# Kernel optimization log

Hardware: AMD Instinct MI355X
Metric: run time of the kernel (lower is better)

Reference implementation:

```python
import jax, jax.numpy as jnp
import numpy as np

B, L, D, M = 8, 2048, 512, 256
D2, H = 2 * D, 4 * D  # attention d_model, FFN hidden
EPS = 1e-6


def setup_inputs() -> dict:
    key = jax.random.key(0)
    ks = jax.random.split(key, 16)
    s2 = 1.0 / np.sqrt(D2)
    sD = 1.0 / np.sqrt(D)
    sH = 1.0 / np.sqrt(H)
    f32 = jnp.float32
    return {
        "zr": jax.random.normal(ks[0], (B, L, D), f32),
        "zi": jax.random.normal(ks[1], (B, L, D), f32),
        "Wq": jax.random.normal(ks[2], (D2, D2), f32) * s2,
        "Wk": jax.random.normal(ks[3], (D2, D2), f32) * s2,
        "Wv": jax.random.normal(ks[4], (D2, D2), f32) * s2,
        "Wo": jax.random.normal(ks[5], (D2, D2), f32) * s2,
        "Wf": jax.random.normal(ks[6], (M, D2), f32),  # trainable random features (std normal, FAVOR+)
        "b_attn": jnp.zeros((D,), f32),
        "W1r": jax.random.normal(ks[7], (D, H), f32) * sD,
        "W1i": jax.random.normal(ks[8], (D, H), f32) * sD,
        "b1r": jnp.zeros((H,), f32),
        "b1i": jnp.zeros((H,), f32),
        "W2r": jax.random.normal(ks[9], (H, D), f32) * sH,
        "W2i": jax.random.normal(ks[10], (H, D), f32) * sH,
        "b2r": jnp.zeros((D,), f32),
        "b2i": jnp.zeros((D,), f32),
        "b_ffn": jnp.zeros((D,), f32),
    }


def modrelu(xr, xi, b):
    # ModReLU: relu(|z| + b) * z / |z|, per-channel bias b
    mag = jnp.sqrt(xr * xr + xi * xi + EPS)
    s = jax.nn.relu(mag + b) / mag
    return xr * s, xi * s


def _block(zr, zi, Wq, Wk, Wv, Wo, Wf, b_attn,
           W1r, W1i, b1r, b1i, W2r, W2i, b2r, b2i, b_ffn):
    # --- kernelized linear attention on real/imag concat [B,L,2D] ---
    x = jnp.concatenate([zr, zi], axis=-1)
    scl = D2 ** -0.25
    q = (x @ Wq) * scl
    k = (x @ Wk) * scl
    v = x @ Wv
    # FAVOR+ positive features: phi(u) = exp(Wf u - |u|^2/2) / sqrt(m)
    pq = q @ Wf.T - 0.5 * jnp.sum(q * q, axis=-1, keepdims=True)  # [B,L,M]
    pk = k @ Wf.T - 0.5 * jnp.sum(k * k, axis=-1, keepdims=True)
    phi_q = jnp.exp(pq - jax.lax.stop_gradient(jnp.max(pq, axis=-1, keepdims=True))) / np.sqrt(M)
    phi_k = jnp.exp(pk - jax.lax.stop_gradient(jnp.max(pk))) / np.sqrt(M)
    kv = jnp.einsum('blm,bld->bmd', phi_k, v)              # [B,M,2D]
    den = jnp.einsum('blm,bm->bl', phi_q, phi_k.sum(axis=1))  # [B,L]
    y = jnp.einsum('blm,bmd->bld', phi_q, kv) / (den[..., None] + EPS)
    y = y @ Wo
    yr, yi = y[..., :D], y[..., D:]
    # Add & Norm (ModReLU)
    zr, zi = modrelu(zr + yr, zi + yi, b_attn)
    # --- complex FFN: complex Linear -> CReLU -> complex Linear ---
    hr = zr @ W1r - zi @ W1i + b1r
    hi = zr @ W1i + zi @ W1r + b1i
    hr = jax.nn.relu(hr)
    hi = jax.nn.relu(hi)
    fr = hr @ W2r - hi @ W2i + b2r
    fi = hr @ W2i + hi @ W2r + b2i
    # Add & Norm (ModReLU)
    zr, zi = modrelu(zr + fr, zi + fi, b_ffn)
    return jnp.stack([zr, zi], axis=-1)  # [B,L,D,2]


def reference(zr, zi, Wq, Wk, Wv, Wo, Wf, b_attn,
              W1r, W1i, b1r, b1i, W2r, W2i, b2r, b2i, b_ffn):
    return _block(zr, zi, Wq, Wk, Wv, Wo, Wf, b_attn,
                  W1r, W1i, b1r, b1i, W2r, W2i, b2r, b2i, b_ffn)
```

## Files before the change

kernel.cpp:

```cpp
#include <hip/hip_runtime.h>
#include <math.h>

#define B_ 8
#define L_ 2048
#define D_ 512
#define M_ 256
#define D2_ 1024
#define H_ 2048
#define N_ 16384
#define EPS_ 1e-6f

typedef __attribute__((ext_vector_type(8))) short bf16x8;
typedef __attribute__((ext_vector_type(4))) float f32x4;
typedef unsigned short ushort_t;
typedef unsigned int uint_t;

#define WAITCNT_VM8 0x0F78
#define WAITCNT_VM6 0x0F76
#define WAITCNT_VM4 0x0F74
#define WAITCNT_VM0 0x0F70

__device__ __forceinline__ ushort_t f2bf(float f) {
    uint_t u = __float_as_uint(f);
    u += 0x7FFFu + ((u >> 16) & 1u);
    return (ushort_t)(u >> 16);
}
__device__ __forceinline__ float bf2f(ushort_t u) {
    return __uint_as_float(((uint_t)u) << 16);
}
__device__ __forceinline__ void gload_lds16(const void* g, void* l) {
    __builtin_amdgcn_global_load_lds(
        (const __attribute__((address_space(1))) void*)g,
        (__attribute__((address_space(3))) void*)l, 16, 0, 0);
}

__global__ __launch_bounds__(256)
void gemm_mfma(const ushort_t* __restrict__ A, const ushort_t* __restrict__ Bm,
               void* __restrict__ Cp, int K, int lda, int ldb, int ldc,
               long long sA, long long sB, long long sC,
               int epi, float alpha, const float* __restrict__ aux,
               int auxStride, const float* __restrict__ bias, int obf)
{
    __shared__ ushort_t As[4][128 * 32];
    __shared__ ushort_t Bs[4][128 * 32];

    const int bz = blockIdx.z;
    A  += (long long)bz * sA;
    Bm += (long long)bz * sB;
    const int row0 = blockIdx.y * 128;
    const int col0 = blockIdx.x * 128;

    const int tid  = threadIdx.x;
    const int lane = tid & 63;
    const int wave = tid >> 6;
    const int wr = wave >> 1, wc = wave & 1;

    const int srow = tid >> 2;
    const int skol = (((tid & 3) ^ ((tid >> 3) & 3)) * 8);

    f32x4 acc[4][4];
    #pragma unroll
    for (int i = 0; i < 4; ++i)
        #pragma unroll
        for (int j = 0; j < 4; ++j)
            acc[i][j] = (f32x4){0.f, 0.f, 0.f, 0.f};

    const int fr = lane & 15;
    const int fq = lane >> 4;
    const int koff = ((fq ^ ((fr >> 1) & 3))) * 8;

    const int nT = K >> 5;

    auto issue = [&](int t) {
        const int buf = t & 3;
        const int k0 = t << 5;
        gload_lds16(A + (long long)(row0 + srow) * lda + k0 + skol,
                    &As[buf][(wave * 16) * 32]);
        gload_lds16(A + (long long)(row0 + 64 + srow) * lda + k0 + skol,
                    &As[buf][(64 + wave * 16) * 32]);
        gload_lds16(Bm + (long long)(col0 + srow) * ldb + k0 + skol,
                    &Bs[buf][(wave * 16) * 32]);
        gload_lds16(Bm + (long long)(col0 + 64 + srow) * ldb + k0 + skol,
                    &Bs[buf][(64 + wave * 16) * 32]);
    };

    issue(0);
    if (nT > 1) issue(1);
    for (int t = 0; t < nT; ++t) {
        if (t + 2 < nT) {
            issue(t + 2);
            __builtin_amdgcn_s_waitcnt(WAITCNT_VM8);
        } else if (t + 1 < nT) {
            __builtin_amdgcn_s_waitcnt(WAITCNT_VM4);
        } else {
            __builtin_amdgcn_s_waitcnt(WAITCNT_VM0);
        }
        __builtin_amdgcn_s_barrier();

        const int cur = t & 3;
        bf16x8 a[4], b[4];
        #pragma unroll
        for (int i = 0; i < 4; ++i)
            a[i] = *(const bf16x8*)&As[cur][(wr * 64 + i * 16 + fr) * 32 + koff];
        #pragma unroll
        for (int j = 0; j < 4; ++j)
            b[j] = *(const bf16x8*)&Bs[cur][(wc * 64 + j * 16 + fr) * 32 + koff];
        #pragma unroll
        for (int i = 0; i < 4; ++i)
            #pragma unroll
            for (int j = 0; j < 4; ++j)
                acc[i][j] = __builtin_amdgcn_mfma_f32_16x16x32_bf16(
                    a[i], b[j], acc[i][j], 0, 0, 0);
    }

    const int gr0 = row0 + wr * 64;
    const int gc0 = col0 + wc * 64;
    #pragma unroll
    for (int i = 0; i < 4; ++i) {
        #pragma unroll
        for (int r = 0; r < 4; ++r) {
            const int row = gr0 + i * 16 + fq * 4 + r;
            float raux = 0.f;
            if (epi == 1 || epi == 2) raux = aux[(long long)bz * auxStride + row];
            #pragma unroll
            for (int j = 0; j < 4; ++j) {
                const int col = gc0 + j * 16 + fr;
                float v = acc[i][j][r];
                if (epi == 0)      v *= alpha;
                else if (epi == 1) v -= 0.5f * raux;
                else if (epi == 2) v = v / (raux + EPS_);
                else if (epi == 5) v -= 0.5f * aux[(long long)bz * auxStride + col];
                else if (epi == 3) { v += bias[col]; v = v > 0.f ? v : 0.f; }
                else if (epi == 4) v += bias[col];
                const long long off = (long long)bz * sC + (long long)row * ldc + col;
                if (obf) ((ushort_t*)Cp)[off] = f2bf(v);
                else     ((float*)Cp)[off] = v;
            }
        }
    }
}

__global__ __launch_bounds__(512, 2)
void gemm256(const ushort_t* __restrict__ A, const ushort_t* __restrict__ Bm,
             void* __restrict__ Cp, int K, int lda, int ldb, int ldc,
             long long sA, long long sB, long long sC,
             int epi, float alpha, const float* __restrict__ aux,
             int auxStride, const float* __restrict__ bias, int obf,
             int ksplit)
{
    __shared__ ushort_t As[2][256 * 64];
    __shared__ ushort_t Bs[2][256 * 64];

    const int bzf = blockIdx.z;
    const int bz = bzf / ksplit;
    const int kz = bzf - bz * ksplit;
    const int Kh = K / ksplit;

    A  += (long long)bz * sA + (long long)kz * Kh;
    Bm += (long long)bz * sB + (long long)kz * Kh;
    const int row0 = blockIdx.y * 256;
    const int col0 = blockIdx.x * 256;

    const int tid  = threadIdx.x;
    const int lane = tid & 63;
    const int wave = tid >> 6;
    const int wr   = wave >> 2;
    const int wcn  = wave & 3;

    const int rloc  = tid >> 3;
    const int csrc8 = (((tid & 7) ^ (rloc & 7)) << 3);

    const int fr = lane & 15;
    const int fq = lane >> 4;
    const int sw = fr & 7;
    const int c0off = ((fq ^ sw) << 3);
    const int c1off = (((4 | fq) ^ sw) << 3);

    const int nT = Kh >> 6;

    f32x4 acc[8][4];
    #pragma unroll
    for (int i = 0; i < 8; ++i)
        #pragma unroll
        for (int j = 0; j < 4; ++j)
            acc[i][j] = (f32x4){0.f, 0.f, 0.f, 0.f};

    bf16x8 a[4][2];
    bf16x8 b[4][2];

    auto stage = [&](int bufS, int tS, int half) {
        const int k0 = tS << 6;
        const int rh = (half >= 2) ? 1 : 0;
        const bool isA = (half == 0 || half == 3);
        const ushort_t* g = isA
            ? A  + (long long)(row0 + rh * 128 + rloc) * lda + k0 + csrc8
            : Bm + (long long)(col0 + rh * 128 + rloc) * ldb + k0 + csrc8;
        const long long gstep = 64LL * (isA ? lda : ldb);
        ushort_t* l = (isA ? &As[bufS][0] : &Bs[bufS][0])
                      + (rh * 128 + wave * 8) * 64;
        gload_lds16(g, l);
        gload_lds16(g + gstep, l + 64 * 64);
    };

    auto ldsA = [&](int buf, int mh, int i, int koff) -> bf16x8 {
        return *(const bf16x8*)
            &As[buf][(wr * 128 + mh * 64 + i * 16 + fr) * 64 + koff];
    };
    auto ldsB = [&](int buf, int j, int koff) -> bf16x8 {
        return *(const bf16x8*)
            &Bs[buf][(wcn * 64 + j * 16 + fr) * 64 + koff];
    };

    stage(0, 0, 0); stage(0, 0, 1); stage(0, 0, 2); stage(0, 0, 3);
    stage(1, 1, 0); stage(1, 1, 1); stage(1, 1, 2); stage(1, 1, 3);
    __builtin_amdgcn_s_waitcnt(WAITCNT_VM8);
    __builtin_amdgcn_s_barrier();

    auto tile_body = [&](int t, int buf) {
        #pragma unroll
        for (int i = 0; i < 4; ++i) {
            a[i][0] = ldsA(buf, 0, i, c0off);
            a[i][1] = ldsA(buf, 0, i, c1off);
        }
        #pragma unroll
        for (int j = 0; j < 2; ++j) {
            b[j][0] = ldsB(buf, j, c0off);
            b[j][1] = ldsB(buf, j, c1off);
        }
        __builtin_amdgcn_s_barrier();
        asm volatile("s_waitcnt lgkmcnt(0)" ::: "memory");
        __builtin_amdgcn_s_setprio(1);
        #pragma unroll
        for (int i = 0; i < 4; ++i)
            #pragma unroll
            for (int j = 0; j < 2; ++j) {
                acc[i][j] = __builtin_amdgcn_mfma_f32_16x16x32_bf16(
                    a[i][0], b[j][0], acc[i][j], 0, 0, 0);
                acc[i][j] = __builtin_amdgcn_mfma_f32_16x16x32_bf16(
                    a[i][1], b[j][1], acc[i][j], 0, 0, 0);
            }
        __builtin_amdgcn_s_setprio(0);
        __builtin_amdgcn_s_barrier();

        #pragma unroll
        for (int j = 2; j < 4; ++j) {
            b[j][0] = ldsB(buf, j, c0off);
            b[j][1] = ldsB(buf, j, c1off);
        }
        __builtin_amdgcn_s_barrier();
        asm volatile("s_waitcnt lgkmcnt(0)" ::: "memory");
        __builtin_amdgcn_s_setprio(1);
        #pragma unroll
        for (int i = 0; i < 4; ++i)
            #pragma unroll
            for (int j = 2; j < 4; ++j) {
                acc[i][j] = __builtin_amdgcn_mfma_f32_16x16x32_bf16(
                    a[i][0], b[j][0], acc[i][j], 0, 0, 0);
                acc[i][j] = __builtin_amdgcn_mfma_f32_16x16x32_bf16(
                    a[i][1], b[j][1], acc[i][j], 0, 0, 0);
            }
        __builtin_amdgcn_s_setprio(0);
        __builtin_amdgcn_s_barrier();

        #pragma unroll
        for (int i = 0; i < 4; ++i) {
            a[i][0] = ldsA(buf, 1, i, c0off);
            a[i][1] = ldsA(buf, 1, i, c1off);
        }
        if (t + 2 < nT) stage(buf, t + 2, 1);
        __builtin_amdgcn_s_barrier();
        asm volatile("s_waitcnt lgkmcnt(0)" ::: "memory");
        __builtin_amdgcn_s_setprio(1);
        #pragma unroll
        for (int i = 0; i < 4; ++i)
            #pragma unroll
            for (int j = 2; j < 4; ++j) {
                acc[4 + i][j] = __builtin_amdgcn_mfma_f32_16x16x32_bf16(
                    a[i][0], b[j][0], acc[4 + i][j], 0, 0, 0);
                acc[4 + i][j] = __builtin_amdgcn_mfma_f32_16x16x32_bf16(
                    a[i][1], b[j][1], acc[4 + i][j], 0, 0, 0);
            }
        __builtin_amdgcn_s_setprio(0);
        __builtin_amdgcn_s_barrier();

        if (t + 2 < nT) {
            stage(buf, t + 2, 2); stage(buf, t + 2, 0); stage(buf, t + 2, 3);
        }
        __builtin_amdgcn_s_barrier();
        asm volatile("s_waitcnt lgkmcnt(0)" ::: "memory");
        __builtin_amdgcn_s_setprio(1);
        #pragma unroll
        for (int i = 0; i < 4; ++i)
            #pragma unroll
            for (int j = 0; j < 2; ++j) {
                acc[4 + i][j] = __builtin_amdgcn_mfma_f32_16x16x32_bf16(
                    a[i][0], b[j][0], acc[4 + i][j], 0, 0, 0);
                acc[4 + i][j] = __builtin_amdgcn_mfma_f32_16x16x32_bf16(
                    a[i][1], b[j][1], acc[4 + i][j], 0, 0, 0);
            }
        __builtin_amdgcn_s_setprio(0);
        if (t + 2 < nT)      __builtin_amdgcn_s_waitcnt(WAITCNT_VM8);
        else if (t + 1 < nT) __builtin_amdgcn_s_waitcnt(WAITCNT_VM0);
        __builtin_amdgcn_s_barrier();
    };

    for (int t = 0; t < nT; t += 2) {
        tile_body(t, 0);
        tile_body(t + 1, 1);
    }

    const int gr0 = row0 + wr * 128;
    const int gc0 = col0 + wcn * 64;
    #pragma unroll
    for (int i = 0; i < 8; ++i) {
        #pragma unroll
        for (int r = 0; r < 4; ++r) {
            const int row = gr0 + i * 16 + fq * 4 + r;
            float raux = 0.f;
            if (epi == 1 || epi == 2) raux = aux[(long long)bz * auxStride + row];
            #pragma unroll
            for (int j = 0; j < 4; ++j) {
                const int col = gc0 + j * 16 + fr;
                float v = acc[i][j][r];
                const long long off = (long long)bz * sC + (long long)row * ldc + col;
                if (ksplit > 1) {
                    atomicAdd((float*)Cp + off, v * alpha);
                    continue;
                }
                if (epi == 0)      v *= alpha;
                else if (epi == 1) v -= 0.5f * raux;
                else if (epi == 2) v = v / (raux + EPS_);
                else if (epi == 5) v -= 0.5f * aux[(long long)bz * auxStride + col];
                else if (epi == 3) { v += bias[col]; v = v > 0.f ? v : 0.f; }
                else if (epi == 4) v += bias[col];
                if (obf) ((ushort_t*)Cp)[off] = f2bf(v);
                else     ((float*)Cp)[off] = v;
            }
        }
    }
}

__global__ __launch_bounds__(256)
void seed_c(const float* __restrict__ bias, float* __restrict__ C)
{
    const long long t = (long long)blockIdx.x * 256 + threadIdx.x;
    C[t] = bias ? bias[(int)(t & (D2_ - 1))] : 0.f;
}


__global__ __launch_bounds__(256)
void transpose_cvt_sq(const float* __restrict__ W, ushort_t* __restrict__ out)
{
    __shared__ float S[32][33];
    const int tx = threadIdx.x & 31, ty = threadIdx.x >> 5;
    const int n0 = blockIdx.x * 32, k0 = blockIdx.y * 32;
    #pragma unroll
    for (int r = 0; r < 4; ++r)
        S[ty + 8 * r][tx] = W[(long long)(k0 + ty + 8 * r) * 1024 + n0 + tx];
    __syncthreads();
    #pragma unroll
    for (int r = 0; r < 4; ++r)
        out[(long long)(n0 + ty + 8 * r) * 1024 + k0 + tx] = f2bf(S[tx][ty + 8 * r]);
}

__global__ __launch_bounds__(256)
void build_wc1T(const float* __restrict__ W1r, const float* __restrict__ W1i,
                ushort_t* __restrict__ out)
{
    __shared__ float S[32][33];
    const int tx = threadIdx.x & 31, ty = threadIdx.x >> 5;
    const int i0 = blockIdx.x * 32, j0 = blockIdx.y * 32;
    #pragma unroll
    for (int r = 0; r < 4; ++r) {
        const int i = i0 + ty + 8 * r, j = j0 + tx;
        float v;
        if (j < H_) v = (i < D_) ? W1r[(long long)i * H_ + j]
                                 : -W1i[(long long)(i - D_) * H_ + j];
        else {
            const int jj = j - H_;
            v = (i < D_) ? W1i[(long long)i * H_ + jj]
                         : W1r[(long long)(i - D_) * H_ + jj];
        }
        S[tx][ty + 8 * r] = v;
    }
    __syncthreads();
    #pragma unroll
    for (int r = 0; r < 4; ++r)
        out[(long long)(j0 + ty + 8 * r) * 1024 + i0 + tx] = f2bf(S[ty + 8 * r][tx]);
}

__global__ __launch_bounds__(256)
void build_wc2T(const float* __restrict__ W2r, const float* __restrict__ W2i,
                ushort_t* __restrict__ out)
{
    __shared__ float S[32][33];
    const int tx = threadIdx.x & 31, ty = threadIdx.x >> 5;
    const int i0 = blockIdx.x * 32, j0 = blockIdx.y * 32;
    #pragma unroll
    for (int r = 0; r < 4; ++r) {
        const int i = i0 + ty + 8 * r, j = j0 + tx;
        float v;
        if (i < H_) v = (j < D_) ? W2r[(long long)i * D_ + j]
                                 : W2i[(long long)i * D_ + (j - D_)];
        else {
            const int ii = i - H_;
            v = (j < D_) ? -W2i[(long long)ii * D_ + j]
                         : W2r[(long long)ii * D_ + (j - D_)];
        }
        S[tx][ty + 8 * r] = v;
    }
    __syncthreads();
    #pragma unroll
    for (int r = 0; r < 4; ++r)
        out[(long long)(j0 + ty + 8 * r) * 4096 + i0 + tx] = f2bf(S[ty + 8 * r][tx]);
}

__global__ __launch_bounds__(256)
void build_bias(const float* __restrict__ b1r, const float* __restrict__ b1i,
                const float* __restrict__ b2r, const float* __restrict__ b2i,
                float* __restrict__ bc1, float* __restrict__ bc2)
{
    const int t = blockIdx.x * 256 + threadIdx.x;
    bc1[t] = (t < H_) ? b1r[t] : b1i[t - H_];
    if (t < D2_) bc2[t] = (t < D_) ? b2r[t] : b2i[t - D_];
}

__global__ __launch_bounds__(256)
void cvt_Wf(const float* __restrict__ Wf, ushort_t* __restrict__ out)
{
    const int t = blockIdx.x * 256 + threadIdx.x;
    out[t] = f2bf(Wf[t]);
}

__global__ __launch_bounds__(256)
void cvt_x(const float* __restrict__ zr, const float* __restrict__ zi,
           ushort_t* __restrict__ x)
{
    long long t = (long long)blockIdx.x * 256 + threadIdx.x;
    long long n = t >> 8;
    int j4 = (int)(t & 255) << 2;
    float4 v;
    if (j4 < D_) v = *(const float4*)(zr + n * D_ + j4);
    else         v = *(const float4*)(zi + n * D_ + (j4 - D_));
    uint2 o;
    o.x = (uint_t)f2bf(v.x) | ((uint_t)f2bf(v.y) << 16);
    o.y = (uint_t)f2bf(v.z) | ((uint_t)f2bf(v.w) << 16);
    *(uint2*)(x + n * D2_ + j4) = o;
}

__global__ __launch_bounds__(256)
void rowsumsq_bf(const ushort_t* __restrict__ A, float* __restrict__ out)
{
    const int wid = threadIdx.x >> 6, lane = threadIdx.x & 63;
    const long long row = (long long)blockIdx.x * 4 + wid;
    const ushort_t* a = A + row * D2_;
    float s = 0.f;
    #pragma unroll
    for (int h = 0; h < 2; ++h) {
        uint4 u = *(const uint4*)(a + h * 512 + lane * 8);
        const uint_t w[4] = {u.x, u.y, u.z, u.w};
        #pragma unroll
        for (int p = 0; p < 4; ++p) {
            float lo = bf2f((ushort_t)(w[p] & 0xffff));
            float hi = bf2f((ushort_t)(w[p] >> 16));
            s += lo * lo + hi * hi;
        }
    }
    #pragma unroll
    for (int off = 32; off; off >>= 1) s += __shfl_down(s, off, 64);
    if (lane == 0) out[row] = s;
}

__global__ __launch_bounds__(256)
void phi_rowmax_exp(const float* __restrict__ P, ushort_t* __restrict__ out)
{
    const long long row = blockIdx.x;
    const int t = threadIdx.x;
    const float v = P[row * M_ + t];
    float m = v;
    #pragma unroll
    for (int off = 32; off; off >>= 1) m = fmaxf(m, __shfl_down(m, off, 64));
    __shared__ float sm[4];
    const int wid = t >> 6, lane = t & 63;
    if (lane == 0) sm[wid] = m;
    __syncthreads();
    const float mm = fmaxf(fmaxf(sm[0], sm[1]), fmaxf(sm[2], sm[3]));
    out[row * M_ + t] = f2bf(expf(v - mm) * 0.0625f);
}

__global__ __launch_bounds__(256)
void gmax1(const float* __restrict__ P, float* __restrict__ part, int n)
{
    float m = -3.4e38f;
    for (long long i = (long long)blockIdx.x * 256 + threadIdx.x; i < n;
         i += (long long)gridDim.x * 256)
        m = fmaxf(m, P[i]);
    #pragma unroll
    for (int off = 32; off; off >>= 1) m = fmaxf(m, __shfl_down(m, off, 64));
    __shared__ float sm[4];
    const int wid = threadIdx.x >> 6, lane = threadIdx.x & 63;
    if (lane == 0) sm[wid] = m;
    __syncthreads();
    if (threadIdx.x == 0)
        part[blockIdx.x] = fmaxf(fmaxf(sm[0], sm[1]), fmaxf(sm[2], sm[3]));
}

__global__ __launch_bounds__(256)
void gmax2(float* __restrict__ red)
{
    float m = -3.4e38f;
    for (int i = threadIdx.x; i < 1024; i += 256) m = fmaxf(m, red[256 + i]);
    #pragma unroll
    for (int off = 32; off; off >>= 1) m = fmaxf(m, __shfl_down(m, off, 64));
    __shared__ float sm[4];
    const int wid = threadIdx.x >> 6, lane = threadIdx.x & 63;
    if (lane == 0) sm[wid] = m;
    __syncthreads();
    if (threadIdx.x == 0) red[0] = fmaxf(fmaxf(sm[0], sm[1]), fmaxf(sm[2], sm[3]));
}

__global__ __launch_bounds__(256)
void phikT_exp(const float* __restrict__ P, const float* __restrict__ red,
               ushort_t* __restrict__ out)
{
    const long long i = (long long)blockIdx.x * 256 + threadIdx.x;
    out[i] = f2bf(expf(P[i] - red[0]) * 0.0625f);
}

__global__ __launch_bounds__(256)
void ksum_k(const ushort_t* __restrict__ phikT, float* __restrict__ ks)
{
    const int b = blockIdx.x >> 8, m = blockIdx.x & 255;
    const ushort_t* p = phikT + (long long)m * N_ + b * L_;
    uint4 u = *(const uint4*)(p + threadIdx.x * 8);
    const uint_t w[4] = {u.x, u.y, u.z, u.w};
    float s = 0.f;
    #pragma unroll
    for (int q = 0; q < 4; ++q)
        s += bf2f((ushort_t)(w[q] & 0xffff)) + bf2f((ushort_t)(w[q] >> 16));
    #pragma unroll
    for (int off = 32; off; off >>= 1) s += __shfl_down(s, off, 64);
    __shared__ float sm[4];
    const int wid = threadIdx.x >> 6, lane = threadIdx.x & 63;
    if (lane == 0) sm[wid] = s;
    __syncthreads();
    if (threadIdx.x == 0)
        ks[blockIdx.x] = sm[0] + sm[1] + sm[2] + sm[3];
}

__global__ __launch_bounds__(256)
void den_k(const ushort_t* __restrict__ phiq, const float* __restrict__ ks,
           float* __restrict__ den)
{
    const int wid = threadIdx.x >> 6, lane = threadIdx.x & 63;
    const long long n = (long long)blockIdx.x * 4 + wid;
    const int b = (int)(n >> 11);
    uint2 u = *(const uint2*)(phiq + n * M_ + lane * 4);
    float4 kk = *(const float4*)(ks + b * M_ + lane * 4);
    float s = bf2f((ushort_t)(u.x & 0xffff)) * kk.x
            + bf2f((ushort_t)(u.x >> 16)) * kk.y
            + bf2f((ushort_t)(u.y & 0xffff)) * kk.z
            + bf2f((ushort_t)(u.y >> 16)) * kk.w;
    #pragma unroll
    for (int off = 32; off; off >>= 1) s += __shfl_down(s, off, 64);
    if (lane == 0) den[n] = s;
}

__global__ __launch_bounds__(256)
void modrelu_attn(const float* __restrict__ zr, const float* __restrict__ zi,
                  const float* __restrict__ yo, const float* __restrict__ b_attn,
                  ushort_t* __restrict__ zst)
{
    const long long t = (long long)blockIdx.x * 256 + threadIdx.x;
    const long long n = t >> 9; const int d = (int)(t & 511);
    const float ar = zr[t] + yo[n * D2_ + d];
    const float ai = zi[t] + yo[n * D2_ + D_ + d];
    const float mag = sqrtf(ar * ar + ai * ai + EPS_);
    const float s = fmaxf(mag + b_attn[d], 0.f) / mag;
    zst[n * D2_ + d]      = f2bf(ar * s);
    zst[n * D2_ + D_ + d] = f2bf(ai * s);
}

__global__ __launch_bounds__(256)
void modrelu_out(const ushort_t* __restrict__ zst, const float* __restrict__ f,
                 const float* __restrict__ b_ffn, float* __restrict__ out)
{
    const long long t = (long long)blockIdx.x * 256 + threadIdx.x;
    const long long n = t >> 9; const int d = (int)(t & 511);
    const float ar = bf2f(zst[n * D2_ + d])      + f[n * D2_ + d];
    const float ai = bf2f(zst[n * D2_ + D_ + d]) + f[n * D2_ + D_ + d];
    const float mag = sqrtf(ar * ar + ai * ai + EPS_);
    const float s = fmaxf(mag + b_ffn[d], 0.f) / mag;
    out[t * 2]     = ar * s;
    out[t * 2 + 1] = ai * s;
}

extern "C" void kernel_launch(void* const* d_in, const int* in_sizes, int n_in,
                              void* d_out, int out_size, void* d_ws, size_t ws_size,
                              hipStream_t stream)
{
    const float* zr    = (const float*)d_in[0];
    const float* zi    = (const float*)d_in[1];
    const float* Wq    = (const float*)d_in[2];
    const float* Wk    = (const float*)d_in[3];
    const float* Wv    = (const float*)d_in[4];
    const float* Wo    = (const float*)d_in[5];
    const float* Wf    = (const float*)d_in[6];
    const float* b_attn= (const float*)d_in[7];
    const float* W1r   = (const float*)d_in[8];
    const float* W1i   = (const float*)d_in[9];
    const float* b1r   = (const float*)d_in[10];
    const float* b1i   = (const float*)d_in[11];
    const float* W2r   = (const float*)d_in[12];
    const float* W2i   = (const float*)d_in[13];
    const float* b2r   = (const float*)d_in[14];
    const float* b2i   = (const float*)d_in[15];
    const float* b_ffn = (const float*)d_in[16];

    char* w = (char*)d_ws;
    ushort_t* Xbf = (ushort_t*)(w + 0LL);
    ushort_t* A1  = (ushort_t*)(w + 33554432LL);
    float*    P   = (float*)   (w + 67108864LL);
    ushort_t* WqT = (ushort_t*)(w + 83886080LL);
    ushort_t* WkT = (ushort_t*)(w + 85983232LL);
    ushort_t* WvT = (ushort_t*)(w + 88080384LL);
    ushort_t* Wfb = (ushort_t*)(w + 90177536LL);
    ushort_t* F1  = (ushort_t*)(w + 100663296LL);
    ushort_t* F2  = (ushort_t*)(w + 109051904LL);
    ushort_t* WoT = (ushort_t*)(w + 117440512LL);
    ushort_t* KVT = (ushort_t*)(w + 119537664LL);
    float* ssqq = (float*)(w + 123731968LL);
    float* ssqk = (float*)(w + 123797504LL);
    float* den  = (float*)(w + 123863040LL);
    float* ksum = (float*)(w + 123928576LL);
    float* red  = (float*)(w + 123936768LL);

    const bool big = ws_size >= 152000000ULL;
    const int  RCH = big ? 8192 : 4096;
    ushort_t* Hb = (ushort_t*)(w + 33554432LL);
    float* Fb  = big ? (float*)(w + 117440512LL) : (float*)(w + 67108864LL);
    float* bc1 = big ? (float*)(w + 150994944LL) : (float*)(w + 123944960LL);
    float* bc2 = big ? (float*)(w + 151011328LL) : (float*)(w + 123961344LL);

    const float scl = 0.1767766952966369f;
    dim3 blk(256);

    auto GM = [&](const ushort_t* A, const ushort_t* Bm, void* C,
                  int rows, int cols, int K, int lda, int ldb, int ldc,
                  long long sA, long long sB, long long sC, int nb,
                  int epi, float alpha, const float* aux, int auxStride,
                  const float* bias, int obf) {
        const long long wg256 = (long long)(cols >> 8) * (rows >> 8) * nb;
        if ((rows & 255) == 0 && (cols & 255) == 0 && (K & 127) == 0 &&
            K >= 512 && wg256 >= 128) {
            dim3 grid(cols / 256, rows / 256, nb);
            gemm256<<<grid, dim3(512), 0, stream>>>(A, Bm, C, K, lda, ldb, ldc,
                                                    sA, sB, sC, epi, alpha, aux,
                                                    auxStride, bias, obf, 1);
        } else {
            dim3 grid(cols / 128, rows / 128, nb);
            gemm_mfma<<<grid, blk, 0, stream>>>(A, Bm, C, K, lda, ldb, ldc,
                                                sA, sB, sC, epi, alpha, aux,
                                                auxStride, bias, obf);
        }
    };

    transpose_cvt_sq<<<dim3(32, 32), blk, 0, stream>>>(Wq, WqT);
    transpose_cvt_sq<<<dim3(32, 32), blk, 0, stream>>>(Wk, WkT);
    transpose_cvt_sq<<<dim3(32, 32), blk, 0, stream>>>(Wv, WvT);
    transpose_cvt_sq<<<dim3(32, 32), blk, 0, stream>>>(Wo, WoT);
    cvt_Wf<<<1024, blk, 0, stream>>>(Wf, Wfb);
    build_bias<<<16, blk, 0, stream>>>(b1r, b1i, b2r, b2i, bc1, bc2);
    cvt_x<<<N_ * (D2_ / 4) / 256, blk, 0, stream>>>(zr, zi, Xbf);

    GM(Xbf, WqT, A1, N_, D2_, D2_, D2_, D2_, D2_, 0, 0, 0, 1, 0, scl, nullptr, 0, nullptr, 1);
    rowsumsq_bf<<<N_ / 4, blk, 0, stream>>>(A1, ssqq);
    GM(A1, Wfb, P, N_, M_, D2_, D2_, D2_, M_, 0, 0, 0, 1, 1, 1.f, ssqq, 0, nullptr, 0);
    phi_rowmax_exp<<<N_, blk, 0, stream>>>(P, F1);

    GM(Xbf, WkT, A1, N_, D2_, D2_, D2_, D2_, D2_, 0, 0, 0, 1, 0, scl, nullptr, 0, nullptr, 1);
    rowsumsq_bf<<<N_ / 4, blk, 0, stream>>>(A1, ssqk);
    GM(Wfb, A1, P, M_, N_, D2_, D2_, D2_, N_, 0, 0, 0, 1, 5, 1.f, ssqk, 0, nullptr, 0);
    gmax1<<<1024, blk, 0, stream>>>(P, red + 256, M_ * N_);
    gmax2<<<1, blk, 0, stream>>>(red);
    phikT_exp<<<M_ * N_ / 256, blk, 0, stream>>>(P, red, F2);

    GM(WvT, Xbf, A1, D2_, N_, D2_, D2_, D2_, N_, 0, 0, 0, 1, 0, 1.f, nullptr, 0, nullptr, 1);

    ksum_k<<<B_ * M_, blk, 0, stream>>>(F2, ksum);
    GM(A1, F2, KVT, D2_, M_, L_, N_, N_, M_, L_, L_, (long long)D2_ * M_, B_,
       0, 1.f, nullptr, 0, nullptr, 1);

    den_k<<<N_ / 4, blk, 0, stream>>>(F1, ksum, den);
    GM(F1, KVT, A1, L_, D2_, M_, M_, M_, D2_, (long long)L_ * M_,
       (long long)D2_ * M_, (long long)L_ * D2_, B_, 2, 1.f, den, L_, nullptr, 1);

    for (int c = 0; c < 2; ++c) {
        const long long ro = (long long)c * 8192;
        GM(A1 + ro * D2_, WoT, P, 8192, D2_, D2_, D2_, D2_, D2_, 0, 0, 0, 1,
           0, 1.f, nullptr, 0, nullptr, 0);
        modrelu_attn<<<8192 * D_ / 256, blk, 0, stream>>>(
            zr + ro * D_, zi + ro * D_, P, b_attn, Xbf + ro * D2_);
    }

    build_wc1T<<<dim3(32, 128), blk, 0, stream>>>(W1r, W1i, F1);
    build_wc2T<<<dim3(128, 32), blk, 0, stream>>>(W2r, W2i, F2);

    for (int c = 0; c < N_ / RCH; ++c) {
        const long long ro = (long long)c * RCH;
        GM(Xbf + ro * D2_, F1, Hb, RCH, 2 * H_, D2_, D2_, D2_, 2 * H_,
           0, 0, 0, 1, 3, 1.f, nullptr, 0, bc1, 1);
        if (RCH == 8192) {
            seed_c<<<RCH * D2_ / 256, blk, 0, stream>>>(bc2, Fb);
            dim3 grid2(D2_ / 256, RCH / 256, 2);
            gemm256<<<grid2, dim3(512), 0, stream>>>(
                Hb, F2, Fb, 2 * H_, 2 * H_, 2 * H_, D2_,
                0, 0, 0, 4, 1.f, nullptr, 0, bc2, 0, 2);
        } else {
            GM(Hb, F2, Fb, RCH, D2_, 2 * H_, 2 * H_, 2 * H_, D2_,
               0, 0, 0, 1, 4, 1.f, nullptr, 0, bc2, 0);
        }
        modrelu_out<<<RCH * D_ / 256, blk, 0, stream>>>(
            Xbf + ro * D2_, Fb, b_ffn, (float*)d_out + ro * D2_);
    }

    (void)in_sizes; (void)n_in; (void)out_size;
}
```

Baseline: 1.148 ms.

## Fold Wo into KV matrix, rebalance GEMM pipelines, and widen gemm256 eligibility

Reassociates the attention output so Wo is multiplied into the small per-batch KV matrix (M x 2D) instead of the full N x 2D attention output. This removes the large post-attention Wo GEMM, and the attention output goes straight into the modrelu kernel in bf16. The small GEMM drops from a 4-stage to a 2-buffer ping-pong with an extra barrier. The 256 GEMM moves one staging load earlier to shrink its prefetch depth, and its K>=512 launch restriction is relaxed. Rounding changes because the product of KV and Wo is now stored in bf16.

Result: faster. 1.063 ms (-7.4%).

```diff
diff --git a/kernel.cpp b/kernel.cpp
--- a/kernel.cpp
+++ b/kernel.cpp
@@ -41,8 +41,8 @@
                int epi, float alpha, const float* __restrict__ aux,
                int auxStride, const float* __restrict__ bias, int obf)
 {
-    __shared__ ushort_t As[4][128 * 32];
-    __shared__ ushort_t Bs[4][128 * 32];
+    __shared__ ushort_t As[2][128 * 32];
+    __shared__ ushort_t Bs[2][128 * 32];
 
     const int bz = blockIdx.z;
     A  += (long long)bz * sA;
@@ -71,46 +71,48 @@
 
     const int nT = K >> 5;
 
-    auto issue = [&](int t) {
-        const int buf = t & 3;
+    auto issue = [&](int t, ushort_t* Ad, ushort_t* Bd) {
         const int k0 = t << 5;
         gload_lds16(A + (long long)(row0 + srow) * lda + k0 + skol,
-                    &As[buf][(wave * 16) * 32]);
+                    Ad + (wave * 16) * 32);
         gload_lds16(A + (long long)(row0 + 64 + srow) * lda + k0 + skol,
-                    &As[buf][(64 + wave * 16) * 32]);
+                    Ad + (64 + wave * 16) * 32);
         gload_lds16(Bm + (long long)(col0 + srow) * ldb + k0 + skol,
-                    &Bs[buf][(wave * 16) * 32]);
+                    Bd + (wave * 16) * 32);
         gload_lds16(Bm + (long long)(col0 + 64 + srow) * ldb + k0 + skol,
-                    &Bs[buf][(64 + wave * 16) * 32]);
+                    Bd + (64 + wave * 16) * 32);
     };
 
-    issue(0);
-    if (nT > 1) issue(1);
-    for (int t = 0; t < nT; ++t) {
-        if (t + 2 < nT) {
-            issue(t + 2);
-            __builtin_amdgcn_s_waitcnt(WAITCNT_VM8);
-        } else if (t + 1 < nT) {
+    auto body = [&](int t, const ushort_t* Ac, const ushort_t* Bc,
+                    ushort_t* An, ushort_t* Bn) {
+        if (t + 1 < nT) {
+            issue(t + 1, An, Bn);
             __builtin_amdgcn_s_waitcnt(WAITCNT_VM4);
         } else {
             __builtin_amdgcn_s_waitcnt(WAITCNT_VM0);
         }
         __builtin_amdgcn_s_barrier();
 
-        const int cur = t & 3;
         bf16x8 a[4], b[4];
         #pragma unroll
         for (int i = 0; i < 4; ++i)
-            a[i] = *(const bf16x8*)&As[cur][(wr * 64 + i * 16 + fr) * 32 + koff];
+            a[i] = *(const bf16x8*)&Ac[(wr * 64 + i * 16 + fr) * 32 + koff];
         #pragma unroll
         for (int j = 0; j < 4; ++j)
-            b[j] = *(const bf16x8*)&Bs[cur][(wc * 64 + j * 16 + fr) * 32 + koff];
+            b[j] = *(const bf16x8*)&Bc[(wc * 64 + j * 16 + fr) * 32 + koff];
         #pragma unroll
         for (int i = 0; i < 4; ++i)
             #pragma unroll
             for (int j = 0; j < 4; ++j)
                 acc[i][j] = __builtin_amdgcn_mfma_f32_16x16x32_bf16(
                     a[i], b[j], acc[i][j], 0, 0, 0);
+        __builtin_amdgcn_s_barrier();
+    };
+
+    issue(0, As[0], Bs[0]);
+    for (int t = 0; t < nT; t += 2) {
+        body(t,     As[0], Bs[0], As[1], Bs[1]);
+        body(t + 1, As[1], Bs[1], As[0], Bs[0]);
     }
 
     const int gr0 = row0 + wr * 64;
@@ -212,8 +214,8 @@
     };
 
     stage(0, 0, 0); stage(0, 0, 1); stage(0, 0, 2); stage(0, 0, 3);
-    stage(1, 1, 0); stage(1, 1, 1); stage(1, 1, 2); stage(1, 1, 3);
-    __builtin_amdgcn_s_waitcnt(WAITCNT_VM8);
+    stage(1, 1, 0); stage(1, 1, 1); stage(1, 1, 2);
+    __builtin_amdgcn_s_waitcnt(WAITCNT_VM6);
     __builtin_amdgcn_s_barrier();
 
     auto tile_body = [&](int t, int buf) {
@@ -227,6 +229,7 @@
             b[j][0] = ldsB(buf, j, c0off);
             b[j][1] = ldsB(buf, j, c1off);
         }
+        if (t + 1 < nT) stage(buf ^ 1, t + 1, 3);
         __builtin_amdgcn_s_barrier();
         asm volatile("s_waitcnt lgkmcnt(0)" ::: "memory");
         __builtin_amdgcn_s_setprio(1);
@@ -283,9 +286,7 @@
         __builtin_amdgcn_s_setprio(0);
         __builtin_amdgcn_s_barrier();
 
-        if (t + 2 < nT) {
-            stage(buf, t + 2, 2); stage(buf, t + 2, 0); stage(buf, t + 2, 3);
-        }
+        if (t + 2 < nT) { stage(buf, t + 2, 2); stage(buf, t + 2, 0); }
         __builtin_amdgcn_s_barrier();
         asm volatile("s_waitcnt lgkmcnt(0)" ::: "memory");
         __builtin_amdgcn_s_setprio(1);
@@ -299,7 +300,7 @@
                     a[i][1], b[j][1], acc[4 + i][j], 0, 0, 0);
             }
         __builtin_amdgcn_s_setprio(0);
-        if (t + 2 < nT)      __builtin_amdgcn_s_waitcnt(WAITCNT_VM8);
+        if (t + 2 < nT)      __builtin_amdgcn_s_waitcnt(WAITCNT_VM6);
         else if (t + 1 < nT) __builtin_amdgcn_s_waitcnt(WAITCNT_VM0);
         __builtin_amdgcn_s_barrier();
     };
@@ -568,13 +569,13 @@
 
 __global__ __launch_bounds__(256)
 void modrelu_attn(const float* __restrict__ zr, const float* __restrict__ zi,
-                  const float* __restrict__ yo, const float* __restrict__ b_attn,
+                  const ushort_t* __restrict__ yo, const float* __restrict__ b_attn,
                   ushort_t* __restrict__ zst)
 {
     const long long t = (long long)blockIdx.x * 256 + threadIdx.x;
     const long long n = t >> 9; const int d = (int)(t & 511);
-    const float ar = zr[t] + yo[n * D2_ + d];
-    const float ai = zi[t] + yo[n * D2_ + D_ + d];
+    const float ar = zr[t] + bf2f(yo[n * D2_ + d]);
+    const float ai = zi[t] + bf2f(yo[n * D2_ + D_ + d]);
     const float mag = sqrtf(ar * ar + ai * ai + EPS_);
     const float s = fmaxf(mag + b_attn[d], 0.f) / mag;
     zst[n * D2_ + d]      = f2bf(ar * s);
@@ -652,7 +653,7 @@
                   const float* bias, int obf) {
         const long long wg256 = (long long)(cols >> 8) * (rows >> 8) * nb;
         if ((rows & 255) == 0 && (cols & 255) == 0 && (K & 127) == 0 &&
-            K >= 512 && wg256 >= 128) {
+            wg256 >= 128) {
             dim3 grid(cols / 256, rows / 256, nb);
             gemm256<<<grid, dim3(512), 0, stream>>>(A, Bm, C, K, lda, ldb, ldc,
                                                     sA, sB, sC, epi, alpha, aux,
@@ -688,20 +689,20 @@
     GM(WvT, Xbf, A1, D2_, N_, D2_, D2_, D2_, N_, 0, 0, 0, 1, 0, 1.f, nullptr, 0, nullptr, 1);
 
     ksum_k<<<B_ * M_, blk, 0, stream>>>(F2, ksum);
-    GM(A1, F2, KVT, D2_, M_, L_, N_, N_, M_, L_, L_, (long long)D2_ * M_, B_,
+    GM(F2, A1, KVT, M_, D2_, L_, N_, N_, D2_, L_, L_, (long long)M_ * D2_, B_,
        0, 1.f, nullptr, 0, nullptr, 1);
 
+    ushort_t* Gb = F2;
+    GM(WoT, KVT, Gb, D2_, M_, D2_, D2_, D2_, M_,
+       0, (long long)M_ * D2_, (long long)D2_ * M_, B_,
+       0, 1.f, nullptr, 0, nullptr, 1);
+
     den_k<<<N_ / 4, blk, 0, stream>>>(F1, ksum, den);
-    GM(F1, KVT, A1, L_, D2_, M_, M_, M_, D2_, (long long)L_ * M_,
+    GM(F1, Gb, P, L_, D2_, M_, M_, M_, D2_, (long long)L_ * M_,
        (long long)D2_ * M_, (long long)L_ * D2_, B_, 2, 1.f, den, L_, nullptr, 1);
 
-    for (int c = 0; c < 2; ++c) {
-        const long long ro = (long long)c * 8192;
-        GM(A1 + ro * D2_, WoT, P, 8192, D2_, D2_, D2_, D2_, D2_, 0, 0, 0, 1,
-           0, 1.f, nullptr, 0, nullptr, 0);
-        modrelu_attn<<<8192 * D_ / 256, blk, 0, stream>>>(
-            zr + ro * D_, zi + ro * D_, P, b_attn, Xbf + ro * D2_);
-    }
+    modrelu_attn<<<N_ * D_ / 256, blk, 0, stream>>>(
+        zr, zi, (const ushort_t*)P, b_attn, Xbf);
 
     build_wc1T<<<dim3(32, 128), blk, 0, stream>>>(W1r, W1i, F1);
     build_wc2T<<<dim3(128, 32), blk, 0, stream>>>(W2r, W2i, F2);
```
